# Kernel tuning notes

Measured on AMD Instinct MI355X. Metric: run time of the kernel, lower is better.

## Reference

```python
import jax, jax.numpy as jnp
import numpy as np

B = 262144
FEATURES = 16
HID = 24
OUT = 784


def setup_inputs() -> dict:
    key = jax.random.key(0)
    ks = jax.random.split(key, 5)
    return {
        "x": jax.random.normal(ks[0], (B, FEATURES), dtype=jnp.float32),
        "W1": jax.random.normal(ks[1], (FEATURES, HID), dtype=jnp.float32) * 0.1,
        "b1": jax.random.normal(ks[2], (HID,), dtype=jnp.float32) * 0.1,
        "W2": jax.random.normal(ks[3], (HID, OUT), dtype=jnp.float32) * 0.1,
        "b2": jax.random.normal(ks[4], (OUT,), dtype=jnp.float32) * 0.1,
    }


def _relu_approx_sigmoid(x):
    # Original: relu(relu(x @ (0.25*I) + (ones-0.5)) @ (-I) + ones) @ (-I) + ones
    # x @ (0.25*I) == 0.25*x ; ones-0.5 == 0.5 ; y @ (-I) == -y.
    # => 1 - relu(1 - relu(0.25*x + 0.5))  (== clamp(0.25*x+0.5, 0, 1))
    a = jax.nn.relu(0.25 * x + 0.5)
    return 1.0 - jax.nn.relu(1.0 - a)


def reference(x, W1, b1, W2, b2):
    h = jax.nn.relu(x @ W1 + b1)          # [B, 24]
    return _relu_approx_sigmoid(h @ W2 + b2)  # [B, 784]
```

## Files before the change

### kernel.cpp

```cpp
#include <hip/hip_runtime.h>


typedef _Float16 h2_t __attribute__((ext_vector_type(2)));

static __device__ __forceinline__ unsigned int pk_h2(float lo, float hi) {
    return __builtin_bit_cast(unsigned int, __builtin_amdgcn_cvt_pkrtz(lo, hi));
}

#if __has_builtin(__builtin_amdgcn_fdot2)
static __device__ __forceinline__ float fdot2u(unsigned int a, unsigned int b, float c) {
    return __builtin_amdgcn_fdot2(__builtin_bit_cast(h2_t, a),
                                  __builtin_bit_cast(h2_t, b), c, false);
}
#else
static __device__ __forceinline__ float fdot2u(unsigned int a, unsigned int b, float c) {
    const h2_t av = __builtin_bit_cast(h2_t, a);
    const h2_t bv = __builtin_bit_cast(h2_t, b);
    return fmaf((float)av.y, (float)bv.y, fmaf((float)av.x, (float)bv.x, c));
}
#endif

#define THREADS 256
#define ROWS_PER_BLOCK 256
#define F 16
#define H 24
#define KP 12
#define NOUT 784
#define NCHUNK (NOUT / 4)

__launch_bounds__(THREADS, 4)
__global__ void decoder_kernel(const float* __restrict__ x,
                               const float* __restrict__ W1,
                               const float* __restrict__ b1,
                               const float* __restrict__ W2,
                               const float* __restrict__ b2,
                               float* __restrict__ out) {
    __shared__ float w1t[H][F];
    __shared__ float b1s[H];
    __shared__ unsigned int hbuf[ROWS_PER_BLOCK][KP];

    const int tid  = threadIdx.x;
    const int row0 = blockIdx.x * ROWS_PER_BLOCK;

    for (int idx = tid; idx < F * H; idx += THREADS) {
        const int i = idx / H, j = idx % H;
        w1t[j][i] = W1[idx];
    }
    if (tid < H) b1s[tid] = b1[tid];

    float4 xv[4];
    {
        const float* xr = x + (size_t)(row0 + tid) * F;
        #pragma unroll
        for (int q = 0; q < 4; ++q)
            xv[q] = *reinterpret_cast<const float4*>(&xr[q * 4]);
    }

    __syncthreads();

    #pragma unroll
    for (int g = 0; g < 3; ++g) {
        float hj[8];
        #pragma unroll
        for (int jj = 0; jj < 8; ++jj) {
            const int j = g * 8 + jj;
            float acc = b1s[j];
            #pragma unroll
            for (int q = 0; q < 4; ++q) {
                const float4 wv = *reinterpret_cast<const float4*>(&w1t[j][q * 4]);
                acc = fmaf(xv[q].x, wv.x, acc);
                acc = fmaf(xv[q].y, wv.y, acc);
                acc = fmaf(xv[q].z, wv.z, acc);
                acc = fmaf(xv[q].w, wv.w, acc);
            }
            hj[jj] = fmaxf(acc, 0.0f);
        }
        uint4 p;
        p.x = pk_h2(hj[0], hj[1]);
        p.y = pk_h2(hj[2], hj[3]);
        p.z = pk_h2(hj[4], hj[5]);
        p.w = pk_h2(hj[6], hj[7]);
        *reinterpret_cast<uint4*>(&hbuf[tid][g * 4]) = p;
    }

    __syncthreads();

    const int cc = (tid < NCHUNK) ? tid : (NCHUNK - 1);
    const int c0 = cc * 4;

    unsigned int w2p[KP][4];
    #pragma unroll
    for (int kp = 0; kp < KP; ++kp) {
        const float4 a = *reinterpret_cast<const float4*>(&W2[(2 * kp + 0) * NOUT + c0]);
        const float4 b = *reinterpret_cast<const float4*>(&W2[(2 * kp + 1) * NOUT + c0]);
        w2p[kp][0] = pk_h2(0.25f * a.x, 0.25f * b.x);
        w2p[kp][1] = pk_h2(0.25f * a.y, 0.25f * b.y);
        w2p[kp][2] = pk_h2(0.25f * a.z, 0.25f * b.z);
        w2p[kp][3] = pk_h2(0.25f * a.w, 0.25f * b.w);
    }
    float4 b2v = *reinterpret_cast<const float4*>(&b2[c0]);
    b2v.x = fmaf(b2v.x, 0.25f, 0.5f);
    b2v.y = fmaf(b2v.y, 0.25f, 0.5f);
    b2v.z = fmaf(b2v.z, 0.25f, 0.5f);
    b2v.w = fmaf(b2v.w, 0.25f, 0.5f);

    if (tid < NCHUNK) {
        float* outp = out + (size_t)row0 * NOUT + c0;
        for (int r = 0; r < ROWS_PER_BLOCK; ++r) {
            const uint4 h0 = *reinterpret_cast<const uint4*>(&hbuf[r][0]);
            const uint4 h1 = *reinterpret_cast<const uint4*>(&hbuf[r][4]);
            const uint4 h2 = *reinterpret_cast<const uint4*>(&hbuf[r][8]);
            unsigned int hw[KP];
            hw[0] = h0.x; hw[1]  = h0.y; hw[2]  = h0.z; hw[3]  = h0.w;
            hw[4] = h1.x; hw[5]  = h1.y; hw[6]  = h1.z; hw[7]  = h1.w;
            hw[8] = h2.x; hw[9]  = h2.y; hw[10] = h2.z; hw[11] = h2.w;

            float4 acc = b2v;
            #pragma unroll
            for (int kp = 0; kp < KP; ++kp) {
                acc.x = fdot2u(hw[kp], w2p[kp][0], acc.x);
                acc.y = fdot2u(hw[kp], w2p[kp][1], acc.y);
                acc.z = fdot2u(hw[kp], w2p[kp][2], acc.z);
                acc.w = fdot2u(hw[kp], w2p[kp][3], acc.w);
            }
            float4 o;
            o.x = fminf(fmaxf(acc.x, 0.f), 1.f);
            o.y = fminf(fmaxf(acc.y, 0.f), 1.f);
            o.z = fminf(fmaxf(acc.z, 0.f), 1.f);
            o.w = fminf(fmaxf(acc.w, 0.f), 1.f);
            *reinterpret_cast<float4*>(outp) = o;
            outp += NOUT;
        }
    }
}

extern "C" void kernel_launch(void* const* d_in, const int* in_sizes, int n_in,
                              void* d_out, int out_size, void* d_ws, size_t ws_size,
                              hipStream_t stream) {
    const float* x  = (const float*)d_in[0];
    const float* W1 = (const float*)d_in[1];
    const float* b1 = (const float*)d_in[2];
    const float* W2 = (const float*)d_in[3];
    const float* b2 = (const float*)d_in[4];
    float* out = (float*)d_out;

    const int B = in_sizes[0] / F;
    const int grid = B / ROWS_PER_BLOCK;
    decoder_kernel<<<grid, THREADS, 0, stream>>>(x, W1, b1, W2, b2, out);
}
```

Before: 183.9 us.

## Compute second layer with MFMA 16x16x32 f16 using shared-memory W2 tiles

Replaces the per-thread fdot2 loop over 256 rows with MFMA f16 matrix instructions: each of 8 waves handles 32 rows and iterates over 49 column tiles of 16, with W2 packed to f16 in LDS (padded to K=32 with zeros). Blocks grow to 512 threads, and every block restages all of W2 into ~50KB of LDS. Output stores become scalar per-lane writes (16 consecutive floats per row segment) instead of float4 stores, which may reduce store efficiency for this write-bound kernel. LDS size and occupancy may also drop.

```diff
diff --git a/kernel.cpp b/kernel.cpp
--- a/kernel.cpp
+++ b/kernel.cpp
@@ -1,32 +1,21 @@
 #include <hip/hip_runtime.h>
 
 
-typedef _Float16 h2_t __attribute__((ext_vector_type(2)));
+typedef _Float16 f16x8 __attribute__((ext_vector_type(8)));
+typedef float    f32x4 __attribute__((ext_vector_type(4)));
+typedef unsigned int u32;
 
-static __device__ __forceinline__ unsigned int pk_h2(float lo, float hi) {
-    return __builtin_bit_cast(unsigned int, __builtin_amdgcn_cvt_pkrtz(lo, hi));
+static __device__ __forceinline__ u32 pk_h2(float lo, float hi) {
+    return __builtin_bit_cast(u32, __builtin_amdgcn_cvt_pkrtz(lo, hi));
 }
 
-#if __has_builtin(__builtin_amdgcn_fdot2)
-static __device__ __forceinline__ float fdot2u(unsigned int a, unsigned int b, float c) {
-    return __builtin_amdgcn_fdot2(__builtin_bit_cast(h2_t, a),
-                                  __builtin_bit_cast(h2_t, b), c, false);
-}
-#else
-static __device__ __forceinline__ float fdot2u(unsigned int a, unsigned int b, float c) {
-    const h2_t av = __builtin_bit_cast(h2_t, a);
-    const h2_t bv = __builtin_bit_cast(h2_t, b);
-    return fmaf((float)av.y, (float)bv.y, fmaf((float)av.x, (float)bv.x, c));
-}
-#endif
-
-#define THREADS 256
-#define ROWS_PER_BLOCK 256
+#define THREADS 512
+#define ROWS 256
 #define F 16
 #define H 24
+#define NOUT 784
+#define NCOLT 49
 #define KP 12
-#define NOUT 784
-#define NCHUNK (NOUT / 4)
 
 __launch_bounds__(THREADS, 4)
 __global__ void decoder_kernel(const float* __restrict__ x,
@@ -37,10 +26,12 @@
                                float* __restrict__ out) {
     __shared__ float w1t[H][F];
     __shared__ float b1s[H];
-    __shared__ unsigned int hbuf[ROWS_PER_BLOCK][KP];
+    __shared__ u32   hbuf[ROWS][16];
+    __shared__ u32   w2b[NOUT][16];
+    __shared__ float b2s[NOUT];
 
     const int tid  = threadIdx.x;
-    const int row0 = blockIdx.x * ROWS_PER_BLOCK;
+    const int row0 = blockIdx.x * ROWS;
 
     for (int idx = tid; idx < F * H; idx += THREADS) {
         const int i = idx / H, j = idx % H;
@@ -48,88 +39,83 @@
     }
     if (tid < H) b1s[tid] = b1[tid];
 
-    float4 xv[4];
-    {
+    for (int c = tid; c < NOUT; c += THREADS)
+        b2s[c] = fmaf(b2[c], 0.25f, 0.5f);
+
+    for (int item = tid; item < NOUT * KP; item += THREADS) {
+        const int col = item / KP, kp = item - col * KP;
+        const float a = W2[(2 * kp + 0) * NOUT + col];
+        const float c = W2[(2 * kp + 1) * NOUT + col];
+        w2b[col][kp] = pk_h2(0.25f * a, 0.25f * c);
+    }
+    for (int item = tid; item < NOUT * 4; item += THREADS) {
+        const int col = item >> 2, kp = 12 + (item & 3);
+        w2b[col][kp] = 0u;
+    }
+
+    if (tid < ROWS) {
+        float4 xv[4];
         const float* xr = x + (size_t)(row0 + tid) * F;
         #pragma unroll
         for (int q = 0; q < 4; ++q)
             xv[q] = *reinterpret_cast<const float4*>(&xr[q * 4]);
+
+        #pragma unroll
+        for (int g = 0; g < 3; ++g) {
+            float hj[8];
+            #pragma unroll
+            for (int jj = 0; jj < 8; ++jj) {
+                const int j = g * 8 + jj;
+                float acc = b1s[j];
+                #pragma unroll
+                for (int q = 0; q < 4; ++q) {
+                    const float4 wv = *reinterpret_cast<const float4*>(&w1t[j][q * 4]);
+                    acc = fmaf(xv[q].x, wv.x, acc);
+                    acc = fmaf(xv[q].y, wv.y, acc);
+                    acc = fmaf(xv[q].z, wv.z, acc);
+                    acc = fmaf(xv[q].w, wv.w, acc);
+                }
+                hj[jj] = fmaxf(acc, 0.0f);
+            }
+            uint4 p;
+            p.x = pk_h2(hj[0], hj[1]);
+            p.y = pk_h2(hj[2], hj[3]);
+            p.z = pk_h2(hj[4], hj[5]);
+            p.w = pk_h2(hj[6], hj[7]);
+            *reinterpret_cast<uint4*>(&hbuf[tid][g * 4]) = p;
+        }
+        *reinterpret_cast<uint4*>(&hbuf[tid][12]) = make_uint4(0u, 0u, 0u, 0u);
     }
 
     __syncthreads();
 
-    #pragma unroll
-    for (int g = 0; g < 3; ++g) {
-        float hj[8];
+    const int wave = tid >> 6;
+    const int lane = tid & 63;
+    const int lg   = lane >> 4;
+    const int lm   = lane & 15;
+
+    const f16x8 a0 = __builtin_bit_cast(f16x8,
+        *reinterpret_cast<const uint4*>(&hbuf[wave * 32 + lm][lg * 4]));
+    const f16x8 a1 = __builtin_bit_cast(f16x8,
+        *reinterpret_cast<const uint4*>(&hbuf[wave * 32 + 16 + lm][lg * 4]));
+
+    float* outp = out + ((size_t)row0 + wave * 32 + lg * 4) * NOUT + lm;
+
+    for (int ct = 0; ct < NCOLT; ++ct) {
+        const int cb = ct * 16;
+        const f16x8 bf = __builtin_bit_cast(f16x8,
+            *reinterpret_cast<const uint4*>(&w2b[cb + lm][lg * 4]));
+        const float bb = b2s[cb + lm];
+        f32x4 acc0 = {bb, bb, bb, bb};
+        f32x4 acc1 = {bb, bb, bb, bb};
+        acc0 = __builtin_amdgcn_mfma_f32_16x16x32_f16(a0, bf, acc0, 0, 0, 0);
+        acc1 = __builtin_amdgcn_mfma_f32_16x16x32_f16(a1, bf, acc1, 0, 0, 0);
+
+        float* p = outp + cb;
         #pragma unroll
-        for (int jj = 0; jj < 8; ++jj) {
-            const int j = g * 8 + jj;
-            float acc = b1s[j];
-            #pragma unroll
-            for (int q = 0; q < 4; ++q) {
-                const float4 wv = *reinterpret_cast<const float4*>(&w1t[j][q * 4]);
-                acc = fmaf(xv[q].x, wv.x, acc);
-                acc = fmaf(xv[q].y, wv.y, acc);
-                acc = fmaf(xv[q].z, wv.z, acc);
-                acc = fmaf(xv[q].w, wv.w, acc);
-            }
-            hj[jj] = fmaxf(acc, 0.0f);
-        }
-        uint4 p;
-        p.x = pk_h2(hj[0], hj[1]);
-        p.y = pk_h2(hj[2], hj[3]);
-        p.z = pk_h2(hj[4], hj[5]);
-        p.w = pk_h2(hj[6], hj[7]);
-        *reinterpret_cast<uint4*>(&hbuf[tid][g * 4]) = p;
-    }
-
-    __syncthreads();
-
-    const int cc = (tid < NCHUNK) ? tid : (NCHUNK - 1);
-    const int c0 = cc * 4;
-
-    unsigned int w2p[KP][4];
-    #pragma unroll
-    for (int kp = 0; kp < KP; ++kp) {
-        const float4 a = *reinterpret_cast<const float4*>(&W2[(2 * kp + 0) * NOUT + c0]);
-        const float4 b = *reinterpret_cast<const float4*>(&W2[(2 * kp + 1) * NOUT + c0]);
-        w2p[kp][0] = pk_h2(0.25f * a.x, 0.25f * b.x);
-        w2p[kp][1] = pk_h2(0.25f * a.y, 0.25f * b.y);
-        w2p[kp][2] = pk_h2(0.25f * a.z, 0.25f * b.z);
-        w2p[kp][3] = pk_h2(0.25f * a.w, 0.25f * b.w);
-    }
-    float4 b2v = *reinterpret_cast<const float4*>(&b2[c0]);
-    b2v.x = fmaf(b2v.x, 0.25f, 0.5f);
-    b2v.y = fmaf(b2v.y, 0.25f, 0.5f);
-    b2v.z = fmaf(b2v.z, 0.25f, 0.5f);
-    b2v.w = fmaf(b2v.w, 0.25f, 0.5f);
-
-    if (tid < NCHUNK) {
-        float* outp = out + (size_t)row0 * NOUT + c0;
-        for (int r = 0; r < ROWS_PER_BLOCK; ++r) {
-            const uint4 h0 = *reinterpret_cast<const uint4*>(&hbuf[r][0]);
-            const uint4 h1 = *reinterpret_cast<const uint4*>(&hbuf[r][4]);
-            const uint4 h2 = *reinterpret_cast<const uint4*>(&hbuf[r][8]);
-            unsigned int hw[KP];
-            hw[0] = h0.x; hw[1]  = h0.y; hw[2]  = h0.z; hw[3]  = h0.w;
-            hw[4] = h1.x; hw[5]  = h1.y; hw[6]  = h1.z; hw[7]  = h1.w;
-            hw[8] = h2.x; hw[9]  = h2.y; hw[10] = h2.z; hw[11] = h2.w;
-
-            float4 acc = b2v;
-            #pragma unroll
-            for (int kp = 0; kp < KP; ++kp) {
-                acc.x = fdot2u(hw[kp], w2p[kp][0], acc.x);
-                acc.y = fdot2u(hw[kp], w2p[kp][1], acc.y);
-                acc.z = fdot2u(hw[kp], w2p[kp][2], acc.z);
-                acc.w = fdot2u(hw[kp], w2p[kp][3], acc.w);
-            }
-            float4 o;
-            o.x = fminf(fmaxf(acc.x, 0.f), 1.f);
-            o.y = fminf(fmaxf(acc.y, 0.f), 1.f);
-            o.z = fminf(fmaxf(acc.z, 0.f), 1.f);
-            o.w = fminf(fmaxf(acc.w, 0.f), 1.f);
-            *reinterpret_cast<float4*>(outp) = o;
-            outp += NOUT;
+        for (int r = 0; r < 4; ++r) {
+            p[(size_t)r * NOUT]        = fminf(fmaxf(acc0[r], 0.f), 1.f);
+            p[(size_t)(16 + r) * NOUT] = fminf(fmaxf(acc1[r], 0.f), 1.f);
         }
     }
 }
@@ -145,6 +131,6 @@
     float* out = (float*)d_out;
 
     const int B = in_sizes[0] / F;
-    const int grid = B / ROWS_PER_BLOCK;
+    const int grid = B / ROWS;
     decoder_kernel<<<grid, THREADS, 0, stream>>>(x, W1, b1, W2, b2, out);
 }
```

Result: slower. 205.8 us (+11.9%).
